# Performance work log

Hardware: AMD Instinct MI355X
Metric: run time of the kernel (lower is better)

The kernel has to match this reference:

```python
import jax, jax.numpy as jnp
import numpy as np

LAMBDA_E_SUM = 10.0
LAMBDA_HIT = 20.0
LAMBDA_CHAMFER = 1e-3
LAMBDA_HIT_ENTROPY = 0.1
EPS = 1e-6
BIG = 1e18


def setup_inputs() -> dict:
    key = jax.random.key(0)
    ks = jax.random.split(key, 7)
    B, Np, Ng, L = 32, 2048, 2048, 256
    pred_feat = jax.random.normal(ks[0], (B, 4, Np), dtype=jnp.float32)
    # hit-probability channel must be in (0,1) (sigmoid head in the real model)
    pred_hit = jax.random.uniform(ks[1], (B, 1, Np), dtype=jnp.float32,
                                  minval=1e-4, maxval=1.0 - 1e-4)
    preds = jnp.concatenate([pred_feat, pred_hit], axis=1)          # [B,5,Np]
    target = jax.random.normal(ks[2], (B, 4, Ng), dtype=jnp.float32)  # [B,4,Ng]
    target_mask = (jax.random.uniform(ks[3], (B, Ng)) < 0.9).astype(jnp.float32)
    mu = jax.random.normal(ks[4], (B, L), dtype=jnp.float32)
    logvar = 0.5 * jax.random.normal(ks[5], (B, L), dtype=jnp.float32)
    e_init = jax.random.uniform(ks[6], (B,), dtype=jnp.float32,
                                minval=10.0, maxval=100.0)
    kl_weight = jnp.float32(1e-3)
    return {"preds": preds, "target": target, "target_mask": target_mask,
            "mu": mu, "logvar": logvar, "e_init": e_init,
            "kl_weight": kl_weight}


def reference(preds, target, target_mask, mu, logvar, e_init, kl_weight):
    B = preds.shape[0]
    preds_t = jnp.swapaxes(preds, 1, 2)    # [B, Np, 5]
    target_t = jnp.swapaxes(target, 1, 2)  # [B, Ng, 4]
    pred_xyz = preds_t[..., :3]            # [B, Np, 3]
    pred_E = preds_t[..., 3]               # [B, Np]
    pred_hit = preds_t[..., 4]             # [B, Np]
    target_xyz = target_t[..., :3]         # [B, Ng, 3]
    target_E = target_t[..., 3]            # [B, Ng]

    # squared pairwise distances [B, Np, Ng]
    pn = jnp.sum(pred_xyz * pred_xyz, axis=-1)      # [B, Np]
    tn = jnp.sum(target_xyz * target_xyz, axis=-1)  # [B, Ng]
    dist_sq = jnp.maximum(
        pn[:, :, None] + tn[:, None, :]
        - 2.0 * jnp.einsum('bnd,bmd->bnm', pred_xyz, target_xyz), 0.0)

    inf_mask = target_mask[:, None, :] == 0.0       # [B, 1->Np, Ng]
    dist_sq_masked = jnp.where(inf_mask, BIG, dist_sq)
    min_dist_pred = jnp.min(dist_sq_masked, axis=2)     # [B, Np]
    idx_pred = jnp.argmin(dist_sq_masked, axis=2)       # [B, Np]
    min_dist_target = jnp.min(dist_sq, axis=1)          # [B, Ng]

    mask_sum = jnp.sum(target_mask)
    loss_chamfer_target = jnp.sum(min_dist_target * target_mask) / mask_sum
    loss_chamfer_pred = jnp.mean(min_dist_pred)
    loss_chamfer = loss_chamfer_target + loss_chamfer_pred

    matched_target_E = jnp.take_along_axis(target_E, idx_pred, axis=1)  # [B, Np]
    loss_local_E = jnp.mean(jnp.abs(pred_E - matched_target_E))

    n_hits_pred = jnp.sum(pred_hit, axis=1)                 # [B]
    n_hits_target = jnp.sum(target_mask, axis=1)            # [B]
    loss_hit_count = jnp.mean((n_hits_pred - n_hits_target) ** 2)

    loss_hit_entropy = -jnp.mean(pred_hit * jnp.log(pred_hit + EPS)
                                 + (1.0 - pred_hit) * jnp.log(1.0 - pred_hit + EPS))

    total_pred_E = jnp.sum(pred_E * pred_hit, axis=1)       # [B]
    loss_global_E_sum = jnp.mean((total_pred_E - e_init) ** 2)

    loss_kld = -0.5 * jnp.sum(1.0 + logvar - mu * mu - jnp.exp(logvar)) / B

    loss_chamf = loss_chamfer * LAMBDA_CHAMFER
    losskld = kl_weight * loss_kld
    loss_global_e = LAMBDA_E_SUM * loss_global_E_sum
    loss_hit = LAMBDA_HIT * loss_hit_count
    loss_hit_entr = LAMBDA_HIT_ENTROPY * loss_hit_entropy

    total_loss = (loss_chamf + loss_local_E + losskld
                  + loss_global_e + loss_hit + loss_hit_entr)
    components = jnp.stack([loss_chamf, loss_local_E, loss_global_e,
                            loss_hit, losskld])
    return total_loss, components
```

## Files before the change

kernel.cpp:

```cpp
#include <hip/hip_runtime.h>

#define BB 32
#define NP 2048
#define NG 2048
#define EPSF 1e-6f
#define BIGF 1e18f
#define FLTMAX 3.4e38f
#define MT 128
#define MP 16
#define TPT 4

#define FPART_OFF 0
#define PPART_OFF 65536
#define TPART_OFF (65536 + BB * MP * NP * 8)

__global__ __launch_bounds__(256, 8) void k_pair(const float* __restrict__ preds,
                                                 const float* __restrict__ target,
                                                 const float* __restrict__ mask,
                                                 unsigned long long* __restrict__ ppart,
                                                 float* __restrict__ tpart) {
  __shared__ float4 s4[MT];
  const int bx = blockIdx.x;
  const int tid = threadIdx.x;

  if (bx < 1024) {
    const int b = bx >> 5;
    const int nch = (bx >> 4) & 1;
    const int mp = bx & 15;
    const float* tb = target + b * 4 * NG;
    const int mbase = mp * MT;
    if (tid < MT) {
      int m = mbase + tid;
      float tx = tb[m], ty = tb[NG + m], tz = tb[2 * NG + m];
      float tn = fmaf(tx, tx, fmaf(ty, ty, tz * tz));
      float w = tn + (mask[b * NG + m] == 0.0f ? BIGF : 0.0f);
      s4[tid] = make_float4(-2.0f * tx, -2.0f * ty, -2.0f * tz, w);
    }
    __syncthreads();

    const float* pb = preds + b * 5 * NP;
    const int nbase = nch * 1024 + tid;
    float px[TPT], py[TPT], pz[TPT], bv[TPT];
    int bi[TPT];
#pragma unroll
    for (int k = 0; k < TPT; k++) {
      int n = nbase + k * 256;
      px[k] = pb[n];
      py[k] = pb[NP + n];
      pz[k] = pb[2 * NP + n];
      bv[k] = FLTMAX;
      bi[k] = 0;
    }

#pragma unroll 4
    for (int m = 0; m < MT; m++) {
      float4 t = s4[m];
#pragma unroll
      for (int k = 0; k < TPT; k++) {
        float s = fmaf(px[k], t.x, fmaf(py[k], t.y, fmaf(pz[k], t.z, t.w)));
        if (s < bv[k]) { bv[k] = s; bi[k] = m; }
      }
    }

    unsigned long long* row = &ppart[(b * MP + mp) * NP];
#pragma unroll
    for (int k = 0; k < TPT; k++) {
      float pn = fmaf(px[k], px[k], fmaf(py[k], py[k], pz[k] * pz[k]));
      float d = fmaxf(bv[k] + pn, 0.0f);
      row[nbase + k * 256] =
          ((unsigned long long)__float_as_uint(d) << 32) | (unsigned)(mbase + bi[k]);
    }
  } else {
    const int bb = bx - 1024;
    const int b = bb >> 5;
    const int mch = (bb >> 4) & 1;
    const int np_ = bb & 15;
    const float* pb = preds + b * 5 * NP;
    if (tid < MT) {
      int n = np_ * MT + tid;
      float px = pb[n], py = pb[NP + n], pz = pb[2 * NP + n];
      float pn2 = fmaf(px, px, fmaf(py, py, pz * pz));
      s4[tid] = make_float4(-2.0f * px, -2.0f * py, -2.0f * pz, pn2);
    }
    __syncthreads();

    const float* tb = target + b * 4 * NG;
    const int mbase2 = mch * 1024 + tid;
    float tx[TPT], ty[TPT], tz[TPT], cv[TPT];
#pragma unroll
    for (int k = 0; k < TPT; k++) {
      int m = mbase2 + k * 256;
      tx[k] = tb[m];
      ty[k] = tb[NG + m];
      tz[k] = tb[2 * NG + m];
      cv[k] = FLTMAX;
    }

#pragma unroll 4
    for (int n = 0; n < MT; n++) {
      float4 p = s4[n];
#pragma unroll
      for (int k = 0; k < TPT; k++)
        cv[k] = fminf(cv[k], fmaf(tx[k], p.x, fmaf(ty[k], p.y, fmaf(tz[k], p.z, p.w))));
    }

    float* row = &tpart[(b * MP + np_) * NG];
#pragma unroll
    for (int k = 0; k < TPT; k++) {
      float tn = fmaf(tx[k], tx[k], fmaf(ty[k], ty[k], tz[k] * tz[k]));
      row[mbase2 + k * 256] = fmaxf(cv[k] + tn, 0.0f);
    }
  }
}

__global__ __launch_bounds__(256) void k_fin(const unsigned long long* __restrict__ ppart,
                                             const float* __restrict__ tpart,
                                             const float* __restrict__ preds,
                                             const float* __restrict__ target,
                                             const float* __restrict__ mask,
                                             const float* __restrict__ mu,
                                             const float* __restrict__ logvar,
                                             float* __restrict__ fpart) {
  __shared__ float red[4][8];
  const int bx = blockIdx.x;
  const int tid = threadIdx.x;
  const int wave = tid >> 6, lane = tid & 63;
  float q0 = 0.0f, q1 = 0.0f, q2 = 0.0f, q3 = 0.0f, q4 = 0.0f;

  if (bx < 128) {
    const int b = bx >> 2;
    const float* pb = preds + b * 5 * NP;
    const float* te = target + b * 4 * NG + 3 * NG;
#pragma unroll
    for (int e = 0; e < 2; e++) {
      int i = bx * 512 + e * 256 + tid;
      int n = i & 2047;
      unsigned long long best = 0xFFFFFFFFFFFFFFFFull;
      const unsigned long long* col = &ppart[b * MP * NP + n];
#pragma unroll
      for (int mp = 0; mp < MP; mp++) {
        unsigned long long v = col[mp * NP];
        best = v < best ? v : best;
      }
      float bd = __uint_as_float((unsigned)(best >> 32));
      int idx = (int)(best & 0xffffffffu);
      float mE = te[idx];
      float pE = pb[3 * NP + n];
      float ph = pb[4 * NP + n];
      q0 += bd;
      q1 += fabsf(pE - mE);
      q2 += ph * logf(ph + EPSF) + (1.0f - ph) * logf(1.0f - ph + EPSF);
      q3 += ph;
      q4 += pE * ph;
    }
  } else if (bx < 256) {
    const int bb = bx - 128;
    const int b = bb >> 2;
#pragma unroll
    for (int e = 0; e < 2; e++) {
      int i = bb * 512 + e * 256 + tid;
      int m = i & 2047;
      float d = FLTMAX;
      const float* col = &tpart[b * MP * NG + m];
#pragma unroll
      for (int np_ = 0; np_ < MP; np_++) d = fminf(d, col[np_ * NG]);
      float msk = mask[i];
      q0 += d * msk;
      q1 += msk;
      q2 += msk;
    }
  } else {
    const int bb = bx - 256;
#pragma unroll
    for (int e = 0; e < 4; e++) {
      int i = bb * 1024 + e * 256 + tid;
      float m = mu[i], lv = logvar[i];
      q0 += 1.0f + lv - m * m - expf(lv);
    }
  }

  float qs[5] = {q0, q1, q2, q3, q4};
  for (int k = 0; k < 5; k++) {
    float v = qs[k];
    v += __shfl_down(v, 32);
    v += __shfl_down(v, 16);
    v += __shfl_down(v, 8);
    v += __shfl_down(v, 4);
    v += __shfl_down(v, 2);
    v += __shfl_down(v, 1);
    if (lane == 0) red[wave][k] = v;
  }
  __syncthreads();
  if (tid < 5) fpart[bx * 8 + tid] = red[0][tid] + red[1][tid] + red[2][tid] + red[3][tid];
}

__global__ __launch_bounds__(256) void k_final(const float* __restrict__ fpart,
                                               const float* __restrict__ e_init,
                                               const float* __restrict__ kl_weight,
                                               float* __restrict__ out) {
  __shared__ float red[4][8];
  const int t = threadIdx.x;
  const int wave = t >> 6, lane = t & 63;
  float g[8] = {0, 0, 0, 0, 0, 0, 0, 0};
  if (t < 128) {
    const float* r = &fpart[t * 8];
    g[0] = r[0]; g[1] = r[1]; g[2] = r[2];
    const float* r2 = &fpart[(128 + t) * 8];
    g[3] = r2[0]; g[4] = r2[1];
  }
  if (t < 8) g[5] = fpart[(256 + t) * 8];
  if (t < BB) {
    float hit = 0.0f, eh = 0.0f, mk = 0.0f;
#pragma unroll
    for (int k = 0; k < 4; k++) {
      hit += fpart[(4 * t + k) * 8 + 3];
      eh += fpart[(4 * t + k) * 8 + 4];
      mk += fpart[(128 + 4 * t + k) * 8 + 2];
    }
    float dh = hit - mk;
    g[6] = dh * dh;
    float de = eh - e_init[t];
    g[7] = de * de;
  }
  for (int k = 0; k < 8; k++) {
    float v = g[k];
    v += __shfl_down(v, 32);
    v += __shfl_down(v, 16);
    v += __shfl_down(v, 8);
    v += __shfl_down(v, 4);
    v += __shfl_down(v, 2);
    v += __shfl_down(v, 1);
    if (lane == 0) red[wave][k] = v;
  }
  __syncthreads();
  if (t == 0) {
    float s[8];
    for (int k = 0; k < 8; k++) s[k] = red[0][k] + red[1][k] + red[2][k] + red[3][k];
    const float invBN = 1.0f / (float)(BB * NP);
    float chamfer_pred = s[0] * invBN;
    float localE = s[1] * invBN;
    float ent = -s[2] * invBN;
    float chamfer_tgt = s[3] / s[4];
    float kld = -0.5f * s[5] / (float)BB;
    float hit = s[6] / (float)BB;
    float ge = s[7] / (float)BB;

    float loss_chamf = (chamfer_tgt + chamfer_pred) * 0.001f;
    float losskld = kl_weight[0] * kld;
    float loss_ge = 10.0f * ge;
    float loss_hit = 20.0f * hit;
    float loss_ent = 0.1f * ent;

    float total = loss_chamf + localE + losskld + loss_ge + loss_hit + loss_ent;
    out[0] = total;
    out[1] = loss_chamf;
    out[2] = localE;
    out[3] = loss_ge;
    out[4] = loss_hit;
    out[5] = losskld;
  }
}

extern "C" void kernel_launch(void* const* d_in, const int* in_sizes, int n_in,
                              void* d_out, int out_size, void* d_ws, size_t ws_size,
                              hipStream_t stream) {
  const float* preds = (const float*)d_in[0];
  const float* target = (const float*)d_in[1];
  const float* mask = (const float*)d_in[2];
  const float* mu = (const float*)d_in[3];
  const float* logvar = (const float*)d_in[4];
  const float* e_init = (const float*)d_in[5];
  const float* kl_weight = (const float*)d_in[6];
  float* fpart = (float*)((char*)d_ws + FPART_OFF);
  unsigned long long* ppart = (unsigned long long*)((char*)d_ws + PPART_OFF);
  float* tpart = (float*)((char*)d_ws + TPART_OFF);
  float* out = (float*)d_out;

  k_pair<<<2048, 256, 0, stream>>>(preds, target, mask, ppart, tpart);
  k_fin<<<264, 256, 0, stream>>>(ppart, tpart, preds, target, mask, mu, logvar, fpart);
  k_final<<<1, 256, 0, stream>>>(fpart, e_init, kl_weight, out);
}
```

Measured before the change: 103.9 us.

## Fuse three kernels into one persistent launch with atomic grid barriers

Merges the pairwise, per-point finalize and final-reduction kernels into a single launch. Global atomic counters with spin-wait barriers replace the kernel boundaries, and a memset resets the counters each call. Work that does not depend on the pairwise results (entropy, hit sums, mask sums, KLD) moves ahead of the first barrier so it overlaps the wait. This removes two launch gaps but relies on the first 264 blocks being co-resident with all 2048 blocks progressing, and it adds spin-wait and memset overhead.

New measurement: 321.5 us. +209.5%, slower.

```diff
diff --git a/kernel.cpp b/kernel.cpp
--- a/kernel.cpp
+++ b/kernel.cpp
@@ -11,17 +11,27 @@
 #define TPT 4
 
 #define FPART_OFF 0
+#define CTR_OFF 16384
 #define PPART_OFF 65536
 #define TPART_OFF (65536 + BB * MP * NP * 8)
 
-__global__ __launch_bounds__(256, 8) void k_pair(const float* __restrict__ preds,
-                                                 const float* __restrict__ target,
-                                                 const float* __restrict__ mask,
-                                                 unsigned long long* __restrict__ ppart,
-                                                 float* __restrict__ tpart) {
+__global__ __launch_bounds__(256, 8) void k_all(const float* __restrict__ preds,
+                                                const float* __restrict__ target,
+                                                const float* __restrict__ mask,
+                                                const float* __restrict__ mu,
+                                                const float* __restrict__ logvar,
+                                                const float* __restrict__ e_init,
+                                                const float* __restrict__ kl_weight,
+                                                unsigned long long* __restrict__ ppart,
+                                                float* __restrict__ tpart,
+                                                float* __restrict__ fpart,
+                                                unsigned* __restrict__ ctr,
+                                                float* __restrict__ out) {
   __shared__ float4 s4[MT];
+  __shared__ float red[4][8];
   const int bx = blockIdx.x;
   const int tid = threadIdx.x;
+  const int wave = tid >> 6, lane = tid & 63;
 
   if (bx < 1024) {
     const int b = bx >> 5;
@@ -51,7 +61,6 @@
       bv[k] = FLTMAX;
       bi[k] = 0;
     }
-
 #pragma unroll 4
     for (int m = 0; m < MT; m++) {
       float4 t = s4[m];
@@ -61,7 +70,6 @@
         if (s < bv[k]) { bv[k] = s; bi[k] = m; }
       }
     }
-
     unsigned long long* row = &ppart[(b * MP + mp) * NP];
 #pragma unroll
     for (int k = 0; k < TPT; k++) {
@@ -95,7 +103,6 @@
       tz[k] = tb[2 * NG + m];
       cv[k] = FLTMAX;
     }
-
 #pragma unroll 4
     for (int n = 0; n < MT; n++) {
       float4 p = s4[n];
@@ -103,7 +110,6 @@
       for (int k = 0; k < TPT; k++)
         cv[k] = fminf(cv[k], fmaf(tx[k], p.x, fmaf(ty[k], p.y, fmaf(tz[k], p.z, p.w))));
     }
-
     float* row = &tpart[(b * MP + np_) * NG];
 #pragma unroll
     for (int k = 0; k < TPT; k++) {
@@ -111,30 +117,58 @@
       row[mbase2 + k * 256] = fmaxf(cv[k] + tn, 0.0f);
     }
   }
-}
-
-__global__ __launch_bounds__(256) void k_fin(const unsigned long long* __restrict__ ppart,
-                                             const float* __restrict__ tpart,
-                                             const float* __restrict__ preds,
-                                             const float* __restrict__ target,
-                                             const float* __restrict__ mask,
-                                             const float* __restrict__ mu,
-                                             const float* __restrict__ logvar,
-                                             float* __restrict__ fpart) {
-  __shared__ float red[4][8];
-  const int bx = blockIdx.x;
-  const int tid = threadIdx.x;
-  const int wave = tid >> 6, lane = tid & 63;
+
+  __threadfence();
+  __syncthreads();
+  if (tid == 0) atomicAdd(&ctr[0], 1u);
+  if (bx >= 264) return;
+
   float q0 = 0.0f, q1 = 0.0f, q2 = 0.0f, q3 = 0.0f, q4 = 0.0f;
-
+  float sv0 = 0.0f, sv1 = 0.0f;
+  float sh0 = 0.0f, sh1 = 0.0f;
   if (bx < 128) {
     const int b = bx >> 2;
     const float* pb = preds + b * 5 * NP;
+    {
+      int n = (bx * 512 + tid) & 2047;
+      sv0 = pb[3 * NP + n];
+      sh0 = pb[4 * NP + n];
+      int n1 = (bx * 512 + 256 + tid) & 2047;
+      sv1 = pb[3 * NP + n1];
+      sh1 = pb[4 * NP + n1];
+    }
+    q2 += sh0 * logf(sh0 + EPSF) + (1.0f - sh0) * logf(1.0f - sh0 + EPSF);
+    q2 += sh1 * logf(sh1 + EPSF) + (1.0f - sh1) * logf(1.0f - sh1 + EPSF);
+    q3 = sh0 + sh1;
+    q4 = sv0 * sh0 + sv1 * sh1;
+  } else if (bx < 256) {
+    const int bb = bx - 128;
+    sv0 = mask[bb * 512 + tid];
+    sv1 = mask[bb * 512 + 256 + tid];
+    q1 = sv0 + sv1;
+    q2 = sv0 + sv1;
+  } else {
+    const int bb = bx - 256;
+#pragma unroll
+    for (int e = 0; e < 4; e++) {
+      int i = bb * 1024 + e * 256 + tid;
+      float m = mu[i], lv = logvar[i];
+      q0 += 1.0f + lv - m * m - expf(lv);
+    }
+  }
+
+  if (tid == 0) {
+    while (atomicAdd(&ctr[0], 0u) < 2048u) __builtin_amdgcn_s_sleep(4);
+  }
+  __syncthreads();
+  __threadfence();
+
+  if (bx < 128) {
+    const int b = bx >> 2;
     const float* te = target + b * 4 * NG + 3 * NG;
 #pragma unroll
     for (int e = 0; e < 2; e++) {
-      int i = bx * 512 + e * 256 + tid;
-      int n = i & 2047;
+      int n = (bx * 512 + e * 256 + tid) & 2047;
       unsigned long long best = 0xFFFFFFFFFFFFFFFFull;
       const unsigned long long* col = &ppart[b * MP * NP + n];
 #pragma unroll
@@ -142,40 +176,21 @@
         unsigned long long v = col[mp * NP];
         best = v < best ? v : best;
       }
-      float bd = __uint_as_float((unsigned)(best >> 32));
-      int idx = (int)(best & 0xffffffffu);
-      float mE = te[idx];
-      float pE = pb[3 * NP + n];
-      float ph = pb[4 * NP + n];
-      q0 += bd;
-      q1 += fabsf(pE - mE);
-      q2 += ph * logf(ph + EPSF) + (1.0f - ph) * logf(1.0f - ph + EPSF);
-      q3 += ph;
-      q4 += pE * ph;
+      q0 += __uint_as_float((unsigned)(best >> 32));
+      float pE = e ? sv1 : sv0;
+      q1 += fabsf(pE - te[(int)(best & 0xffffffffu)]);
     }
   } else if (bx < 256) {
     const int bb = bx - 128;
     const int b = bb >> 2;
 #pragma unroll
     for (int e = 0; e < 2; e++) {
-      int i = bb * 512 + e * 256 + tid;
-      int m = i & 2047;
+      int m = (bb * 512 + e * 256 + tid) & 2047;
       float d = FLTMAX;
       const float* col = &tpart[b * MP * NG + m];
 #pragma unroll
       for (int np_ = 0; np_ < MP; np_++) d = fminf(d, col[np_ * NG]);
-      float msk = mask[i];
-      q0 += d * msk;
-      q1 += msk;
-      q2 += msk;
-    }
-  } else {
-    const int bb = bx - 256;
-#pragma unroll
-    for (int e = 0; e < 4; e++) {
-      int i = bb * 1024 + e * 256 + tid;
-      float m = mu[i], lv = logvar[i];
-      q0 += 1.0f + lv - m * m - expf(lv);
+      q0 += d * (e ? sv1 : sv0);
     }
   }
 
@@ -192,34 +207,36 @@
   }
   __syncthreads();
   if (tid < 5) fpart[bx * 8 + tid] = red[0][tid] + red[1][tid] + red[2][tid] + red[3][tid];
-}
-
-__global__ __launch_bounds__(256) void k_final(const float* __restrict__ fpart,
-                                               const float* __restrict__ e_init,
-                                               const float* __restrict__ kl_weight,
-                                               float* __restrict__ out) {
-  __shared__ float red[4][8];
-  const int t = threadIdx.x;
-  const int wave = t >> 6, lane = t & 63;
+  __threadfence();
+  __syncthreads();
+  if (tid == 0) atomicAdd(&ctr[1], 1u);
+  if (bx != 0) return;
+
+  if (tid == 0) {
+    while (atomicAdd(&ctr[1], 0u) < 264u) __builtin_amdgcn_s_sleep(4);
+  }
+  __syncthreads();
+  __threadfence();
+
   float g[8] = {0, 0, 0, 0, 0, 0, 0, 0};
-  if (t < 128) {
-    const float* r = &fpart[t * 8];
+  if (tid < 128) {
+    const float* r = &fpart[tid * 8];
     g[0] = r[0]; g[1] = r[1]; g[2] = r[2];
-    const float* r2 = &fpart[(128 + t) * 8];
+    const float* r2 = &fpart[(128 + tid) * 8];
     g[3] = r2[0]; g[4] = r2[1];
   }
-  if (t < 8) g[5] = fpart[(256 + t) * 8];
-  if (t < BB) {
+  if (tid < 8) g[5] = fpart[(256 + tid) * 8];
+  if (tid < BB) {
     float hit = 0.0f, eh = 0.0f, mk = 0.0f;
 #pragma unroll
     for (int k = 0; k < 4; k++) {
-      hit += fpart[(4 * t + k) * 8 + 3];
-      eh += fpart[(4 * t + k) * 8 + 4];
-      mk += fpart[(128 + 4 * t + k) * 8 + 2];
+      hit += fpart[(4 * tid + k) * 8 + 3];
+      eh += fpart[(4 * tid + k) * 8 + 4];
+      mk += fpart[(128 + 4 * tid + k) * 8 + 2];
     }
     float dh = hit - mk;
     g[6] = dh * dh;
-    float de = eh - e_init[t];
+    float de = eh - e_init[tid];
     g[7] = de * de;
   }
   for (int k = 0; k < 8; k++) {
@@ -233,7 +250,7 @@
     if (lane == 0) red[wave][k] = v;
   }
   __syncthreads();
-  if (t == 0) {
+  if (tid == 0) {
     float s[8];
     for (int k = 0; k < 8; k++) s[k] = red[0][k] + red[1][k] + red[2][k] + red[3][k];
     const float invBN = 1.0f / (float)(BB * NP);
@@ -272,11 +289,12 @@
   const float* e_init = (const float*)d_in[5];
   const float* kl_weight = (const float*)d_in[6];
   float* fpart = (float*)((char*)d_ws + FPART_OFF);
+  unsigned* ctr = (unsigned*)((char*)d_ws + CTR_OFF);
   unsigned long long* ppart = (unsigned long long*)((char*)d_ws + PPART_OFF);
   float* tpart = (float*)((char*)d_ws + TPART_OFF);
   float* out = (float*)d_out;
 
-  k_pair<<<2048, 256, 0, stream>>>(preds, target, mask, ppart, tpart);
-  k_fin<<<264, 256, 0, stream>>>(ppart, tpart, preds, target, mask, mu, logvar, fpart);
-  k_final<<<1, 256, 0, stream>>>(fpart, e_init, kl_weight, out);
+  hipMemsetAsync(ctr, 0, 2 * sizeof(unsigned), stream);
+  k_all<<<2048, 256, 0, stream>>>(preds, target, mask, mu, logvar, e_init,
+                                  kl_weight, ppart, tpart, fpart, ctr, out);
 }
```
